# Performance work log

Measured on AMD Instinct MI355X. Metric: run time of the kernel, lower is better.

Reference implementation:

```python
import jax, jax.numpy as jnp
import numpy as np


def _masked(scores, mask):
    return jnp.where(mask == 0, -jnp.inf, scores)


def setup_inputs() -> dict:
    key = jax.random.key(0)
    ks = jax.random.split(key, 4)
    B, H, S, D = 2, 12, 4096, 64
    blk = 64
    nb = S // blk          # 64 blocks
    nw = nb - 2            # 62 windows
    R = 3                  # random blocks per window
    return {
        'query': jax.random.normal(ks[0], (B, H, S, D), dtype=jnp.float32),
        'key': jax.random.normal(ks[1], (B, H, S, D), dtype=jnp.float32),
        'value': jax.random.normal(ks[2], (B, H, S, D), dtype=jnp.float32),
        'q_mask': jnp.ones((B, 1, S, 1), dtype=jnp.float32),
        'kv_mask': jnp.ones((B, 1, 1, S), dtype=jnp.float32),
        'band_mask': jnp.ones((B, 1, nb - 4, blk, 3 * blk), dtype=jnp.float32),
        'q_block_mask': jnp.ones((B, nb, blk), dtype=jnp.float32),
        'kv_block_mask': jnp.ones((B, nb, blk), dtype=jnp.float32),
        'random_attn': jax.random.randint(ks[3], (H, nw, R), 0, nb, dtype=jnp.int32),
        'q_block_size': blk,
        'kv_block_size': blk,
    }


def reference(query, key, value, q_mask, kv_mask, band_mask, q_block_mask,
              kv_block_mask, random_attn, q_block_size, kv_block_size):
    B, H, S, D = query.shape
    Skv = key.shape[2]
    qb, kb = q_block_size, kv_block_size
    nb, nkb = S // qb, Skv // kb
    scale = 1.0 / (D ** 0.5)

    # expand random indices over batch: [B,H,nw,R]
    ra = jnp.broadcast_to(random_attn[None].astype(jnp.int32),
                          (B,) + random_attn.shape)
    nw, R = ra.shape[2], ra.shape[3]
    bidx = jnp.arange(B)[:, None, None, None]
    hidx = jnp.arange(H)[None, :, None, None]

    # random mask: [B,H,nw,qb,R*kb]
    rm = kv_block_mask[bidx, ra].reshape(B, H, nw, R * kb)
    random_mask = jnp.einsum('blq,bhlk->bhlqk', q_block_mask[:, 1:-1], rm)

    bq = query.reshape(B, H, nb, qb, D)
    bk = key.reshape(B, H, nkb, kb, D)
    bv = value.reshape(B, H, nkb, kb, D)

    # gathered random blocks: [B,H,nw,R*kb,D]
    sk = bk[bidx, hidx, ra].reshape(B, H, nw, R * kb, D)
    sv = bv[bidx, hidx, ra].reshape(B, H, nw, R * kb, D)

    # --- first query block: attends to everything ---
    p1 = jnp.einsum('bhqd,bhkd->bhqk', bq[:, :, 0], key) * scale
    a1 = jax.nn.softmax(_masked(p1, kv_mask), axis=-1)
    c1 = jnp.einsum('bhqk,bhkd->bhqd', a1, value)[:, :, None]

    # --- second query block ---
    k2 = jnp.concatenate([bk[:, :, 0], bk[:, :, 1], bk[:, :, 2], bk[:, :, -1],
                          sk[:, :, 0]], axis=2)
    v2 = jnp.concatenate([bv[:, :, 0], bv[:, :, 1], bv[:, :, 2], bv[:, :, -1],
                          sv[:, :, 0]], axis=2)
    p2 = jnp.einsum('bhqd,bhkd->bhqk', bq[:, :, 1], k2) * scale
    seq_pad = jnp.concatenate([kv_mask[:, :, :, :3 * kb],
                               kv_mask[:, :, :, -kb:],
                               jnp.ones_like(random_mask[:, :1, 0, :1])], axis=3)
    rand_pad = jnp.concatenate([jnp.ones_like(p2[:, :, :, :4 * kb]),
                                random_mask[:, :, 0]], axis=3)
    a2 = jax.nn.softmax(_masked(p2, jnp.minimum(seq_pad, rand_pad)), axis=-1)
    c2 = jnp.einsum('bhqk,bhkd->bhqd', a2, v2)[:, :, None]

    # --- middle blocks: window + global(first,last) + random ---
    ebk = jnp.concatenate([bk[:, :, 1:-3], bk[:, :, 2:-2], bk[:, :, 3:-1]], axis=3)
    ebv = jnp.concatenate([bv[:, :, 1:-3], bv[:, :, 2:-2], bv[:, :, 3:-1]], axis=3)
    mq = bq[:, :, 2:-2]  # [B,H,nb-4,qb,D]
    inner = _masked(jnp.einsum('bhlqd,bhlkd->bhlqk', mq, ebk) * scale, band_mask)
    randp = _masked(jnp.einsum('bhlqd,bhlkd->bhlqk', mq, sk[:, :, 1:-1]) * scale,
                    random_mask[:, :, 1:-1])
    fop = _masked(jnp.einsum('bhlqd,bhkd->bhlqk', mq, bk[:, :, 0]) * scale,
                  kv_mask[:, :, :, :kb][:, :, :, None, :])
    lop = _masked(jnp.einsum('bhlqd,bhkd->bhlqk', mq, bk[:, :, -1]) * scale,
                  kv_mask[:, :, :, -kb:][:, :, :, None, :])
    band = jnp.concatenate([fop, inner, lop, randp], axis=-1)
    aw = jax.nn.softmax(band, axis=-1)
    cm = jnp.einsum('bhlqk,bhlkd->bhlqd', aw[..., kb:4 * kb], ebv)
    cm += jnp.einsum('bhlqk,bhlkd->bhlqd', aw[..., 4 * kb:-kb], sv[:, :, 1:-1])
    cm += jnp.einsum('bhlqk,bhkd->bhlqd', aw[..., :kb], bv[:, :, 0])
    cm += jnp.einsum('bhlqk,bhkd->bhlqd', aw[..., -kb:], bv[:, :, -1])

    # --- second-to-last query block ---
    k3 = jnp.concatenate([bk[:, :, 0], bk[:, :, -3], bk[:, :, -2], bk[:, :, -1],
                          sk[:, :, -1]], axis=2)
    v3 = jnp.concatenate([bv[:, :, 0], bv[:, :, -3], bv[:, :, -2], bv[:, :, -1],
                          sv[:, :, -1]], axis=2)
    p3 = jnp.einsum('bhqd,bhkd->bhqk', bq[:, :, -2], k3) * scale
    seq_pad3 = jnp.concatenate([kv_mask[:, :, :, :kb],
                                kv_mask[:, :, :, -3 * kb:],
                                jnp.ones_like(random_mask[:, :1, 0, :1])], axis=3)
    rand_pad3 = jnp.concatenate([jnp.ones_like(p3[:, :, :, :4 * kb]),
                                 random_mask[:, :, -1]], axis=3)
    a3 = jax.nn.softmax(_masked(p3, jnp.minimum(seq_pad3, rand_pad3)), axis=-1)
    c3 = jnp.einsum('bhqk,bhkd->bhqd', a3, v3)[:, :, None]

    # --- last query block: attends to everything ---
    p4 = jnp.einsum('bhqd,bhkd->bhqk', bq[:, :, -1], key) * scale
    a4 = jax.nn.softmax(_masked(p4, kv_mask), axis=-1)
    c4 = jnp.einsum('bhqk,bhkd->bhqd', a4, value)[:, :, None]

    ctx = jnp.concatenate([c1, c2, cm, c3, c4], axis=2)
    return ctx.reshape(B, H, S, D) * q_mask
```

## Files before the change

### kernel.cpp

```cpp
#include <hip/hip_runtime.h>
#include <hip/hip_bf16.h>

#define BB 2
#define HH 12
#define SS 4096
#define DD 64
#define NB_ 64
#define NW_ 62
#define RR 3

#define PARTIAL_FLOATS 4160
#define N_HEAVY_UNITS  (BB * HH * 2)
#define N_CHUNKS       8
#define N_TILES        (BB * HH * NB_)
#define TILE_ELEMS     4096

using short8 = __attribute__((ext_vector_type(8))) short;
using f32x4  = __attribute__((ext_vector_type(4))) float;

__device__ __forceinline__ int swz(int r, int c) {
    return (r << 6) + ((((c >> 3) ^ r) & 7) << 3) + (c & 7);
}

__device__ __forceinline__ short pack_bf16(float f) {
    __bf16 b = (__bf16)f;
    return (short)__builtin_bit_cast(unsigned short, b);
}

__device__ __forceinline__ short8 load_cvt8_scaled(const float* p, float sc) {
    f32x4 a = *(const f32x4*)p;
    f32x4 b = *(const f32x4*)(p + 4);
    short8 r;
#pragma unroll
    for (int i = 0; i < 4; ++i) {
        r[i]     = pack_bf16(a[i] * sc);
        r[i + 4] = pack_bf16(b[i] * sc);
    }
    return r;
}

__device__ __forceinline__ void dma16(const short* gsrc, short* lds) {
    __builtin_amdgcn_global_load_lds(
        (const __attribute__((address_space(1))) void*)gsrc,
        (__attribute__((address_space(3))) void*)lds, 16, 0, 0);
}

__global__ __launch_bounds__(256)
void bigbird_prepass(const float* __restrict__ K, const float* __restrict__ V,
                     short* __restrict__ Kimg, short* __restrict__ Vimg)
{
    const int tile = blockIdx.x;
    const int tid  = threadIdx.x;
    const size_t gbase = (size_t)tile * TILE_ELEMS;

    {
        const int kr = tid >> 2, kc = (tid & 3) * 16;
        const float* kp = K + gbase + kr * 64 + kc;
        f32x4 a0 = *(const f32x4*)(kp);
        f32x4 a1 = *(const f32x4*)(kp + 4);
        f32x4 a2 = *(const f32x4*)(kp + 8);
        f32x4 a3 = *(const f32x4*)(kp + 12);
        short8 s0, s1;
#pragma unroll
        for (int i = 0; i < 4; ++i) {
            s0[i] = pack_bf16(a0[i]); s0[i + 4] = pack_bf16(a1[i]);
            s1[i] = pack_bf16(a2[i]); s1[i + 4] = pack_bf16(a3[i]);
        }
        short* kt = Kimg + gbase;
        *(short8*)&kt[swz(kr, kc)]     = s0;
        *(short8*)&kt[swz(kr, kc + 8)] = s1;
    }
    {
        const int vp = tid & 31, vd = (tid >> 5) * 8;
        const float* v0 = V + gbase + (2 * vp) * 64 + vd;
        f32x4 b0 = *(const f32x4*)(v0);
        f32x4 b1 = *(const f32x4*)(v0 + 4);
        f32x4 c0 = *(const f32x4*)(v0 + 64);
        f32x4 c1 = *(const f32x4*)(v0 + 64 + 4);
        short* vt = Vimg + gbase;
#pragma unroll
        for (int i = 0; i < 8; ++i) {
            float f0 = (i < 4) ? b0[i] : b1[i - 4];
            float f1 = (i < 4) ? c0[i] : c1[i - 4];
            unsigned int pk = (unsigned int)(unsigned short)pack_bf16(f0) |
                              ((unsigned int)(unsigned short)pack_bf16(f1) << 16);
            *(unsigned int*)&vt[swz(vd + i, 2 * vp)] = pk;
        }
    }
}

__global__ __launch_bounds__(256, 4)
void bigbird_main_img(const short* __restrict__ Kimg, const short* __restrict__ Vimg,
                      const float* __restrict__ Q, const float* __restrict__ qmask,
                      const int* __restrict__ ra, float* __restrict__ Out,
                      float* __restrict__ part)
{
    __shared__ __align__(16) short KB[2][TILE_ELEMS];
    __shared__ __align__(16) short VT[2][TILE_ELEMS];
    __shared__ __align__(16) short PB[4][16 * 64];

    const int tid  = threadIdx.x;
    const int w    = tid >> 6;
    const int lane = tid & 63;
    const int g    = lane >> 4;
    const int m    = lane & 15;

    const int idx    = blockIdx.x;
    const int NHEAVY = N_HEAVY_UNITS * N_CHUNKS;

    bool heavy;
    int  b, h, qb, u = 0, chunk_base = 0, chunk = 0, nlist;
    int  slist[8], vlist[8];

    if (idx < NHEAVY) {
        heavy = true;
        u = idx >> 3; chunk = idx & 7; chunk_base = chunk * 8; nlist = 8;
        const int bh = u >> 1;
        b = bh / HH; h = bh % HH;
        qb = (u & 1) ? (NB_ - 1) : 0;
    } else {
        heavy = false;
        const int idx2 = idx - NHEAVY;
        const int qidx = idx2 / (BB * HH);
        const int bh   = idx2 % (BB * HH);
        b = bh / HH; h = bh % HH;
        qb = qidx + 1;
        const int* rp = ra + (h * NW_ + (qb - 1)) * RR;
        if (qb == 1) {
            slist[0] = 0; slist[1] = 1; slist[2] = 2; slist[3] = 63;
            slist[4] = rp[0]; slist[5] = rp[1]; slist[6] = rp[2]; nlist = 7;
#pragma unroll
            for (int i = 0; i < 7; ++i) vlist[i] = slist[i];
        } else if (qb == NB_ - 2) {
            slist[0] = 0; slist[1] = 61; slist[2] = 62; slist[3] = 63;
            slist[4] = rp[0]; slist[5] = rp[1]; slist[6] = rp[2]; nlist = 7;
#pragma unroll
            for (int i = 0; i < 7; ++i) vlist[i] = slist[i];
        } else {
            slist[0] = 0; slist[1] = qb - 1; slist[2] = qb; slist[3] = qb + 1;
            slist[4] = 63; slist[5] = rp[0]; slist[6] = rp[1]; slist[7] = rp[2];
            vlist[0] = 0; vlist[1] = qb - 1; vlist[2] = qb; vlist[3] = qb + 1;
            vlist[4] = rp[0]; vlist[5] = rp[1]; vlist[6] = rp[2]; vlist[7] = 63;
            nlist = 8;
        }
    }

    const int    bh_lin = b * HH + h;
    const size_t base   = (size_t)bh_lin * SS * DD;
    const short* Kbh    = Kimg + (size_t)bh_lin * NB_ * TILE_ELEMS;
    const short* Vbh    = Vimg + (size_t)bh_lin * NB_ * TILE_ELEMS;

    short8 qa[2];
    {
        const float* qp = Q + base + (size_t)(qb * 64 + w * 16 + m) * DD + g * 8;
        qa[0] = load_cvt8_scaled(qp, 0.125f);
        qa[1] = load_cvt8_scaled(qp + 32, 0.125f);
    }

    f32x4 oacc[4];
#pragma unroll
    for (int t = 0; t < 4; ++t) oacc[t] = (f32x4){0.f, 0.f, 0.f, 0.f};
    float lsum[4] = {0.f, 0.f, 0.f, 0.f};

    const int c0 = w * 2;
    auto issue = [&](int buf, int i) {
        const int kbs = heavy ? (chunk_base + i) : slist[i];
        const int kbv = heavy ? (chunk_base + i) : vlist[i];
        const short* sk = Kbh + (size_t)kbs * TILE_ELEMS + (lane << 3);
        const short* sv = Vbh + (size_t)kbv * TILE_ELEMS + (lane << 3);
#pragma unroll
        for (int i2 = 0; i2 < 2; ++i2) {
            dma16(sk + (c0 + i2) * 512, &KB[buf][(c0 + i2) * 512]);
            dma16(sv + (c0 + i2) * 512, &VT[buf][(c0 + i2) * 512]);
        }
    };

    issue(0, 0);
    int cur = 0;

    for (int it = 0; it < nlist; ++it) {
        __syncthreads();

        if (it + 1 < nlist) issue(cur ^ 1, it + 1);

        f32x4 sacc[4];
#pragma unroll
        for (int t = 0; t < 4; ++t) sacc[t] = (f32x4){0.f, 0.f, 0.f, 0.f};
        __builtin_amdgcn_s_setprio(1);
#pragma unroll
        for (int ks = 0; ks < 2; ++ks) {
#pragma unroll
            for (int t = 0; t < 4; ++t) {
                short8 bk = *(short8*)&KB[cur][swz(t * 16 + m, g * 8 + ks * 32)];
                sacc[t] = __builtin_amdgcn_mfma_f32_16x16x32_bf16(qa[ks], bk, sacc[t], 0, 0, 0);
            }
        }
        __builtin_amdgcn_s_setprio(0);

#pragma unroll
        for (int t = 0; t < 4; ++t) {
#pragma unroll
            for (int j = 0; j < 4; ++j) {
                const float p = __expf(sacc[t][j]);
                lsum[j] += p;
                PB[w][swz(4 * g + j, t * 16 + m)] = pack_bf16(p);
            }
        }

        __builtin_amdgcn_s_setprio(1);
#pragma unroll
        for (int ks = 0; ks < 2; ++ks) {
            short8 pa = *(short8*)&PB[w][swz(m, g * 8 + ks * 32)];
#pragma unroll
            for (int t = 0; t < 4; ++t) {
                short8 bv = *(short8*)&VT[cur][swz(t * 16 + m, g * 8 + ks * 32)];
                oacc[t] = __builtin_amdgcn_mfma_f32_16x16x32_bf16(pa, bv, oacc[t], 0, 0, 0);
            }
        }
        __builtin_amdgcn_s_setprio(0);

        cur ^= 1;
    }

#pragma unroll
    for (int j = 0; j < 4; ++j)
#pragma unroll
        for (int off = 1; off < 16; off <<= 1) lsum[j] += __shfl_xor(lsum[j], off);

    if (heavy) {
        float* pb = part + (size_t)(u * N_CHUNKS + chunk) * PARTIAL_FLOATS;
#pragma unroll
        for (int j = 0; j < 4; ++j) {
            const int row = w * 16 + 4 * g + j;
#pragma unroll
            for (int t = 0; t < 4; ++t) pb[row * 64 + t * 16 + m] = oacc[t][j];
            if (m == 0) pb[4096 + row] = lsum[j];
        }
    } else {
#pragma unroll
        for (int j = 0; j < 4; ++j) {
            const int row = qb * 64 + w * 16 + 4 * g + j;
            const float sc = qmask[b * SS + row] / lsum[j];
            float* op = Out + base + (size_t)row * DD + m;
#pragma unroll
            for (int t = 0; t < 4; ++t) op[t * 16] = oacc[t][j] * sc;
        }
    }
}

template<bool SPLIT>
__global__ __launch_bounds__(256)
void bigbird_main_reg(const float* __restrict__ Q, const float* __restrict__ K,
                      const float* __restrict__ V, const float* __restrict__ qmask,
                      const int* __restrict__ ra, float* __restrict__ Out,
                      float* __restrict__ ws)
{
    __shared__ __align__(16) short KB[2][64 * 64];
    __shared__ __align__(16) short VT[2][64 * 64];
    __shared__ __align__(16) short PB[4][16 * 64];

    const int tid  = threadIdx.x;
    const int w    = tid >> 6;
    const int lane = tid & 63;
    const int g    = lane >> 4;
    const int m    = lane & 15;

    const int idx    = blockIdx.x;
    const int NHEAVY = SPLIT ? (N_HEAVY_UNITS * N_CHUNKS) : N_HEAVY_UNITS;

    bool heavy;
    int  b, h, qb, u = 0, chunk = 0, chunk_base = 0, nlist;
    int  slist[8], vlist[8];

    if (idx < NHEAVY) {
        heavy = true;
        if (SPLIT) { u = idx >> 3; chunk = idx & 7; chunk_base = chunk * 8; nlist = 8; }
        else       { u = idx; chunk_base = 0; nlist = NB_; }
        const int bh = u >> 1;
        b = bh / HH; h = bh % HH;
        qb = (u & 1) ? (NB_ - 1) : 0;
    } else {
        heavy = false;
        const int idx2 = idx - NHEAVY;
        const int qidx = idx2 / (BB * HH);
        const int bh   = idx2 % (BB * HH);
        b = bh / HH; h = bh % HH;
        qb = qidx + 1;
        const int* rp = ra + (h * NW_ + (qb - 1)) * RR;
        if (qb == 1) {
            slist[0] = 0; slist[1] = 1; slist[2] = 2; slist[3] = 63;
            slist[4] = rp[0]; slist[5] = rp[1]; slist[6] = rp[2]; nlist = 7;
#pragma unroll
            for (int i = 0; i < 7; ++i) vlist[i] = slist[i];
        } else if (qb == NB_ - 2) {
            slist[0] = 0; slist[1] = 61; slist[2] = 62; slist[3] = 63;
            slist[4] = rp[0]; slist[5] = rp[1]; slist[6] = rp[2]; nlist = 7;
#pragma unroll
            for (int i = 0; i < 7; ++i) vlist[i] = slist[i];
        } else {
            slist[0] = 0; slist[1] = qb - 1; slist[2] = qb; slist[3] = qb + 1;
            slist[4] = 63; slist[5] = rp[0]; slist[6] = rp[1]; slist[7] = rp[2];
            vlist[0] = 0; vlist[1] = qb - 1; vlist[2] = qb; vlist[3] = qb + 1;
            vlist[4] = rp[0]; vlist[5] = rp[1]; vlist[6] = rp[2]; vlist[7] = 63;
            nlist = 8;
        }
    }

    const size_t base = ((size_t)(b * HH + h)) * SS * DD;

    short8 qa[2];
    {
        const float* qp = Q + base + (size_t)(qb * 64 + w * 16 + m) * DD + g * 8;
        qa[0] = load_cvt8_scaled(qp, 0.125f);
        qa[1] = load_cvt8_scaled(qp + 32, 0.125f);
    }

    f32x4 oacc[4];
#pragma unroll
    for (int t = 0; t < 4; ++t) oacc[t] = (f32x4){0.f, 0.f, 0.f, 0.f};
    float lsum[4] = {0.f, 0.f, 0.f, 0.f};

    const int kr = tid >> 2;
    const int kc = (tid & 3) * 16;
    const int vp = tid & 31;
    const int vd = (tid >> 5) * 8;

    f32x4 kreg[4], vreg[4];
    auto load_kv = [&](int i) {
        const int kbs = heavy ? (chunk_base + i) : slist[i];
        const int kbv = heavy ? (chunk_base + i) : vlist[i];
        const float* kp = K + base + (size_t)(kbs * 64 + kr) * DD + kc;
        kreg[0] = *(const f32x4*)(kp);
        kreg[1] = *(const f32x4*)(kp + 4);
        kreg[2] = *(const f32x4*)(kp + 8);
        kreg[3] = *(const f32x4*)(kp + 12);
        const float* vp0 = V + base + (size_t)(kbv * 64 + 2 * vp) * DD + vd;
        vreg[0] = *(const f32x4*)(vp0);
        vreg[1] = *(const f32x4*)(vp0 + 4);
        vreg[2] = *(const f32x4*)(vp0 + DD);
        vreg[3] = *(const f32x4*)(vp0 + DD + 4);
    };

    load_kv(0);
    int cur = 0;

    for (int it = 0; it < nlist; ++it) {
        {
            short8 s0, s1;
#pragma unroll
            for (int i = 0; i < 4; ++i) {
                s0[i] = pack_bf16(kreg[0][i]); s0[i + 4] = pack_bf16(kreg[1][i]);
                s1[i] = pack_bf16(kreg[2][i]); s1[i + 4] = pack_bf16(kreg[3][i]);
            }
            *(short8*)&KB[cur][swz(kr, kc)]     = s0;
            *(short8*)&KB[cur][swz(kr, kc + 8)] = s1;
#pragma unroll
            for (int i = 0; i < 8; ++i) {
                float f0 = (i < 4) ? vreg[0][i] : vreg[1][i - 4];
                float f1 = (i < 4) ? vreg[2][i] : vreg[3][i - 4];
                unsigned int pk = (unsigned int)(unsigned short)pack_bf16(f0) |
                                  ((unsigned int)(unsigned short)pack_bf16(f1) << 16);
                *(unsigned int*)&VT[cur][swz(vd + i, 2 * vp)] = pk;
            }
        }

        __syncthreads();

        if (it + 1 < nlist) load_kv(it + 1);

        f32x4 sacc[4];
#pragma unroll
        for (int t = 0; t < 4; ++t) sacc[t] = (f32x4){0.f, 0.f, 0.f, 0.f};
        __builtin_amdgcn_s_setprio(1);
#pragma unroll
        for (int ks = 0; ks < 2; ++ks) {
#pragma unroll
            for (int t = 0; t < 4; ++t) {
                short8 bk = *(short8*)&KB[cur][swz(t * 16 + m, g * 8 + ks * 32)];
                sacc[t] = __builtin_amdgcn_mfma_f32_16x16x32_bf16(qa[ks], bk, sacc[t], 0, 0, 0);
            }
        }
        __builtin_amdgcn_s_setprio(0);

#pragma unroll
        for (int t = 0; t < 4; ++t) {
#pragma unroll
            for (int j = 0; j < 4; ++j) {
                const float p = __expf(sacc[t][j]);
                lsum[j] += p;
                PB[w][swz(4 * g + j, t * 16 + m)] = pack_bf16(p);
            }
        }

        __builtin_amdgcn_s_setprio(1);
#pragma unroll
        for (int ks = 0; ks < 2; ++ks) {
            short8 pa = *(short8*)&PB[w][swz(m, g * 8 + ks * 32)];
#pragma unroll
            for (int t = 0; t < 4; ++t) {
                short8 bv = *(short8*)&VT[cur][swz(t * 16 + m, g * 8 + ks * 32)];
                oacc[t] = __builtin_amdgcn_mfma_f32_16x16x32_bf16(pa, bv, oacc[t], 0, 0, 0);
            }
        }
        __builtin_amdgcn_s_setprio(0);

        cur ^= 1;
    }

#pragma unroll
    for (int j = 0; j < 4; ++j)
#pragma unroll
        for (int off = 1; off < 16; off <<= 1) lsum[j] += __shfl_xor(lsum[j], off);

    if (SPLIT && heavy) {
        float* pb = ws + (size_t)(u * N_CHUNKS + chunk) * PARTIAL_FLOATS;
#pragma unroll
        for (int j = 0; j < 4; ++j) {
            const int row = w * 16 + 4 * g + j;
#pragma unroll
            for (int t = 0; t < 4; ++t) pb[row * 64 + t * 16 + m] = oacc[t][j];
            if (m == 0) pb[4096 + row] = lsum[j];
        }
    } else {
#pragma unroll
        for (int j = 0; j < 4; ++j) {
            const int row = qb * 64 + w * 16 + 4 * g + j;
            const float sc = qmask[b * SS + row] / lsum[j];
            float* op = Out + base + (size_t)row * DD + m;
#pragma unroll
            for (int t = 0; t < 4; ++t) op[t * 16] = oacc[t][j] * sc;
        }
    }
}

__global__ __launch_bounds__(256)
void bigbird_combine(const float* __restrict__ ws, const float* __restrict__ qmask,
                     float* __restrict__ Out)
{
    const int u  = blockIdx.x;
    const int bh = u >> 1;
    const int b  = bh / HH;
    const int h  = bh % HH;
    const int qb = (u & 1) ? (NB_ - 1) : 0;

    const int tid = threadIdx.x;
    const int r   = tid >> 2;
    const int s   = tid & 3;

    const float* pb0 = ws + (size_t)u * N_CHUNKS * PARTIAL_FLOATS;

    float L = 0.f;
    f32x4 o0 = {0,0,0,0}, o1 = {0,0,0,0}, o2 = {0,0,0,0}, o3 = {0,0,0,0};
#pragma unroll
    for (int c = 0; c < N_CHUNKS; ++c) {
        const float* pb = pb0 + c * PARTIAL_FLOATS;
        L += pb[4096 + r];
        const float* orow = pb + r * 64 + s * 16;
        f32x4 a0 = *(const f32x4*)(orow);
        f32x4 a1 = *(const f32x4*)(orow + 4);
        f32x4 a2 = *(const f32x4*)(orow + 8);
        f32x4 a3 = *(const f32x4*)(orow + 12);
#pragma unroll
        for (int i = 0; i < 4; ++i) {
            o0[i] += a0[i]; o1[i] += a1[i];
            o2[i] += a2[i]; o3[i] += a3[i];
        }
    }

    const int row = qb * 64 + r;
    const float scme = qmask[b * SS + row] / L;
    float* op = Out + ((size_t)(b * HH + h)) * SS * DD + (size_t)row * DD + s * 16;
#pragma unroll
    for (int i = 0; i < 4; ++i) { o0[i] *= scme; o1[i] *= scme; o2[i] *= scme; o3[i] *= scme; }
    *(f32x4*)(op)      = o0;
    *(f32x4*)(op + 4)  = o1;
    *(f32x4*)(op + 8)  = o2;
    *(f32x4*)(op + 12) = o3;
}

extern "C" void kernel_launch(void* const* d_in, const int* in_sizes, int n_in,
                              void* d_out, int out_size, void* d_ws, size_t ws_size,
                              hipStream_t stream) {
    const float* Q     = (const float*)d_in[0];
    const float* K     = (const float*)d_in[1];
    const float* V     = (const float*)d_in[2];
    const float* qmask = (const float*)d_in[3];
    const int*   ra    = (const int*)d_in[8];
    float* Out = (float*)d_out;

    const size_t img_bytes  = (size_t)N_TILES * TILE_ELEMS * sizeof(short);
    const size_t part_bytes = (size_t)N_HEAVY_UNITS * N_CHUNKS * PARTIAL_FLOATS * sizeof(float);
    const size_t need_img   = 2 * img_bytes + part_bytes;

    if (ws_size >= need_img) {
        short* Kimg = (short*)d_ws;
        short* Vimg = Kimg + (size_t)N_TILES * TILE_ELEMS;
        float* part = (float*)((char*)d_ws + 2 * img_bytes);
        bigbird_prepass<<<N_TILES, 256, 0, stream>>>(K, V, Kimg, Vimg);
        const int grid = N_HEAVY_UNITS * N_CHUNKS + BB * HH * (NB_ - 2);
        bigbird_main_img<<<grid, 256, 0, stream>>>(Kimg, Vimg, Q, qmask, ra, Out, part);
        bigbird_combine<<<N_HEAVY_UNITS, 256, 0, stream>>>((const float*)part, qmask, Out);
    } else if (ws_size >= part_bytes) {
        float* ws = (float*)d_ws;
        const int grid = N_HEAVY_UNITS * N_CHUNKS + BB * HH * (NB_ - 2);
        bigbird_main_reg<true><<<grid, 256, 0, stream>>>(Q, K, V, qmask, ra, Out, ws);
        bigbird_combine<<<N_HEAVY_UNITS, 256, 0, stream>>>((const float*)ws, qmask, Out);
    } else {
        float* ws = (float*)d_ws;
        const int grid = N_HEAVY_UNITS + BB * HH * (NB_ - 2);
        bigbird_main_reg<false><<<grid, 256, 0, stream>>>(Q, K, V, qmask, ra, Out, ws);
    }
}
```

Before: 58.21 us.

## Split KV tiles into 32-key half-slices to shrink LDS and raise occupancy

Each 64-key K/V tile is now processed as two 32-key halves. The V image is re-laid out per half with a new 32-column swizzle, and the LDS buffers for K, V and P are halved. The per-block slist/vlist arrays become lambdas computed from three random indices, and launch bounds go from 4 to 6 blocks per SM. The aim is higher occupancy through lower LDS and register use, at the cost of twice as many barrier-separated iterations, each doing less MFMA work.

```diff
diff --git a/kernel.cpp b/kernel.cpp
--- a/kernel.cpp
+++ b/kernel.cpp
@@ -20,6 +20,9 @@
 
 __device__ __forceinline__ int swz(int r, int c) {
     return (r << 6) + ((((c >> 3) ^ r) & 7) << 3) + (c & 7);
+}
+__device__ __forceinline__ int swz32(int r, int c) {
+    return (r << 5) + ((((c >> 3) ^ r ^ (r >> 2)) & 3) << 3) + (c & 7);
 }
 
 __device__ __forceinline__ short pack_bf16(float f) {
@@ -72,32 +75,35 @@
     }
     {
         const int vp = tid & 31, vd = (tid >> 5) * 8;
-        const float* v0 = V + gbase + (2 * vp) * 64 + vd;
+        const int key  = 2 * vp;
+        const int half = key >> 5;
+        const int kp2  = key & 31;
+        const float* v0 = V + gbase + key * 64 + vd;
         f32x4 b0 = *(const f32x4*)(v0);
         f32x4 b1 = *(const f32x4*)(v0 + 4);
         f32x4 c0 = *(const f32x4*)(v0 + 64);
         f32x4 c1 = *(const f32x4*)(v0 + 64 + 4);
-        short* vt = Vimg + gbase;
+        short* vt = Vimg + gbase + half * 2048;
 #pragma unroll
         for (int i = 0; i < 8; ++i) {
             float f0 = (i < 4) ? b0[i] : b1[i - 4];
             float f1 = (i < 4) ? c0[i] : c1[i - 4];
             unsigned int pk = (unsigned int)(unsigned short)pack_bf16(f0) |
                               ((unsigned int)(unsigned short)pack_bf16(f1) << 16);
-            *(unsigned int*)&vt[swz(vd + i, 2 * vp)] = pk;
-        }
-    }
-}
-
-__global__ __launch_bounds__(256, 4)
+            *(unsigned int*)&vt[swz32(vd + i, kp2)] = pk;
+        }
+    }
+}
+
+__global__ __launch_bounds__(256, 6)
 void bigbird_main_img(const short* __restrict__ Kimg, const short* __restrict__ Vimg,
                       const float* __restrict__ Q, const float* __restrict__ qmask,
                       const int* __restrict__ ra, float* __restrict__ Out,
                       float* __restrict__ part)
 {
-    __shared__ __align__(16) short KB[2][TILE_ELEMS];
-    __shared__ __align__(16) short VT[2][TILE_ELEMS];
-    __shared__ __align__(16) short PB[4][16 * 64];
+    __shared__ __align__(16) short KB[2][2048];
+    __shared__ __align__(16) short VT[2][2048];
+    __shared__ __align__(16) short PB[4][512];
 
     const int tid  = threadIdx.x;
     const int w    = tid >> 6;
@@ -110,7 +116,7 @@
 
     bool heavy;
     int  b, h, qb, u = 0, chunk_base = 0, chunk = 0, nlist;
-    int  slist[8], vlist[8];
+    int  r0 = 0, r1 = 0, r2 = 0;
 
     if (idx < NHEAVY) {
         heavy = true;
@@ -126,24 +132,27 @@
         b = bh / HH; h = bh % HH;
         qb = qidx + 1;
         const int* rp = ra + (h * NW_ + (qb - 1)) * RR;
-        if (qb == 1) {
-            slist[0] = 0; slist[1] = 1; slist[2] = 2; slist[3] = 63;
-            slist[4] = rp[0]; slist[5] = rp[1]; slist[6] = rp[2]; nlist = 7;
-#pragma unroll
-            for (int i = 0; i < 7; ++i) vlist[i] = slist[i];
-        } else if (qb == NB_ - 2) {
-            slist[0] = 0; slist[1] = 61; slist[2] = 62; slist[3] = 63;
-            slist[4] = rp[0]; slist[5] = rp[1]; slist[6] = rp[2]; nlist = 7;
-#pragma unroll
-            for (int i = 0; i < 7; ++i) vlist[i] = slist[i];
-        } else {
-            slist[0] = 0; slist[1] = qb - 1; slist[2] = qb; slist[3] = qb + 1;
-            slist[4] = 63; slist[5] = rp[0]; slist[6] = rp[1]; slist[7] = rp[2];
-            vlist[0] = 0; vlist[1] = qb - 1; vlist[2] = qb; vlist[3] = qb + 1;
-            vlist[4] = rp[0]; vlist[5] = rp[1]; vlist[6] = rp[2]; vlist[7] = 63;
-            nlist = 8;
-        }
-    }
+        r0 = rp[0]; r1 = rp[1]; r2 = rp[2];
+        nlist = (qb == 1 || qb == NB_ - 2) ? 7 : 8;
+    }
+
+    auto kb_s = [&](int ti) -> int {
+        if (heavy) return chunk_base + ti;
+        if (qb == 1)
+            return ti == 0 ? 0 : ti == 1 ? 1 : ti == 2 ? 2 : ti == 3 ? 63
+                 : ti == 4 ? r0 : ti == 5 ? r1 : r2;
+        if (qb == NB_ - 2)
+            return ti == 0 ? 0 : ti == 1 ? 61 : ti == 2 ? 62 : ti == 3 ? 63
+                 : ti == 4 ? r0 : ti == 5 ? r1 : r2;
+        return ti == 0 ? 0 : ti == 1 ? qb - 1 : ti == 2 ? qb : ti == 3 ? qb + 1
+             : ti == 4 ? 63 : ti == 5 ? r0 : ti == 6 ? r1 : r2;
+    };
+    auto kb_v = [&](int ti) -> int {
+        if (heavy) return chunk_base + ti;
+        if (qb == 1 || qb == NB_ - 2) return kb_s(ti);
+        return ti == 0 ? 0 : ti == 1 ? qb - 1 : ti == 2 ? qb : ti == 3 ? qb + 1
+             : ti == 4 ? r0 : ti == 5 ? r1 : ti == 6 ? r2 : 63;
+    };
 
     const int    bh_lin = b * HH + h;
     const size_t base   = (size_t)bh_lin * SS * DD;
@@ -162,59 +171,56 @@
     for (int t = 0; t < 4; ++t) oacc[t] = (f32x4){0.f, 0.f, 0.f, 0.f};
     float lsum[4] = {0.f, 0.f, 0.f, 0.f};
 
-    const int c0 = w * 2;
-    auto issue = [&](int buf, int i) {
-        const int kbs = heavy ? (chunk_base + i) : slist[i];
-        const int kbv = heavy ? (chunk_base + i) : vlist[i];
-        const short* sk = Kbh + (size_t)kbs * TILE_ELEMS + (lane << 3);
-        const short* sv = Vbh + (size_t)kbv * TILE_ELEMS + (lane << 3);
-#pragma unroll
-        for (int i2 = 0; i2 < 2; ++i2) {
-            dma16(sk + (c0 + i2) * 512, &KB[buf][(c0 + i2) * 512]);
-            dma16(sv + (c0 + i2) * 512, &VT[buf][(c0 + i2) * 512]);
-        }
+    auto issue = [&](int buf, int sl) {
+        const int ti = sl >> 1, half = sl & 1;
+        const short* sk = Kbh + (size_t)kb_s(ti) * TILE_ELEMS + half * 2048
+                        + w * 512 + (lane << 3);
+        const short* sv = Vbh + (size_t)kb_v(ti) * TILE_ELEMS + half * 2048
+                        + w * 512 + (lane << 3);
+        dma16(sk, &KB[buf][w * 512]);
+        dma16(sv, &VT[buf][w * 512]);
     };
 
+    const int nslice = nlist * 2;
     issue(0, 0);
     int cur = 0;
 
-    for (int it = 0; it < nlist; ++it) {
+    for (int sl = 0; sl < nslice; ++sl) {
         __syncthreads();
 
-        if (it + 1 < nlist) issue(cur ^ 1, it + 1);
-
-        f32x4 sacc[4];
-#pragma unroll
-        for (int t = 0; t < 4; ++t) sacc[t] = (f32x4){0.f, 0.f, 0.f, 0.f};
+        if (sl + 1 < nslice) issue(cur ^ 1, sl + 1);
+
+        f32x4 sacc[2];
+        sacc[0] = (f32x4){0.f, 0.f, 0.f, 0.f};
+        sacc[1] = (f32x4){0.f, 0.f, 0.f, 0.f};
         __builtin_amdgcn_s_setprio(1);
 #pragma unroll
         for (int ks = 0; ks < 2; ++ks) {
 #pragma unroll
-            for (int t = 0; t < 4; ++t) {
-                short8 bk = *(short8*)&KB[cur][swz(t * 16 + m, g * 8 + ks * 32)];
-                sacc[t] = __builtin_amdgcn_mfma_f32_16x16x32_bf16(qa[ks], bk, sacc[t], 0, 0, 0);
+            for (int kt = 0; kt < 2; ++kt) {
+                short8 bk = *(short8*)&KB[cur][swz(kt * 16 + m, g * 8 + ks * 32)];
+                sacc[kt] = __builtin_amdgcn_mfma_f32_16x16x32_bf16(qa[ks], bk, sacc[kt], 0, 0, 0);
             }
         }
         __builtin_amdgcn_s_setprio(0);
 
 #pragma unroll
-        for (int t = 0; t < 4; ++t) {
+        for (int t = 0; t < 2; ++t) {
 #pragma unroll
             for (int j = 0; j < 4; ++j) {
                 const float p = __expf(sacc[t][j]);
                 lsum[j] += p;
-                PB[w][swz(4 * g + j, t * 16 + m)] = pack_bf16(p);
+                PB[w][swz32(4 * g + j, t * 16 + m)] = pack_bf16(p);
             }
         }
 
         __builtin_amdgcn_s_setprio(1);
-#pragma unroll
-        for (int ks = 0; ks < 2; ++ks) {
-            short8 pa = *(short8*)&PB[w][swz(m, g * 8 + ks * 32)];
-#pragma unroll
-            for (int t = 0; t < 4; ++t) {
-                short8 bv = *(short8*)&VT[cur][swz(t * 16 + m, g * 8 + ks * 32)];
-                oacc[t] = __builtin_amdgcn_mfma_f32_16x16x32_bf16(pa, bv, oacc[t], 0, 0, 0);
+        {
+            short8 pa = *(short8*)&PB[w][swz32(m, g * 8)];
+#pragma unroll
+            for (int dt = 0; dt < 4; ++dt) {
+                short8 bv = *(short8*)&VT[cur][swz32(dt * 16 + m, g * 8)];
+                oacc[dt] = __builtin_amdgcn_mfma_f32_16x16x32_bf16(pa, bv, oacc[dt], 0, 0, 0);
             }
         }
         __builtin_amdgcn_s_setprio(0);
```

Measured after the change: 65.22 us. 12.0% more time.
